# Performance work log

Hardware: AMD Instinct MI355X
Metric: run time of the kernel (lower is better)

The kernel has to match this reference:

```python
import jax, jax.numpy as jnp
import numpy as np

B, T, IN_F, OUT_F = 2, 1024, 1024, 4096
CHUNK = 64  # out_features chunk to bound the (N, CHUNK, IN_F) intermediate


def setup_inputs() -> dict:
    key = jax.random.key(0)
    k1, k2 = jax.random.split(key)
    x = jax.random.normal(k1, (B, T, IN_F), dtype=jnp.float32)
    # torch reset_parameters: uniform_(-0.1, 0.1)
    w = jax.random.uniform(k2, (OUT_F, IN_F), minval=-0.1, maxval=0.1, dtype=jnp.float32)
    b = jnp.zeros((OUT_F,), dtype=jnp.float32)  # bias initialized to zeros
    return {"input": x, "weight_patterns": w, "bias": b}


def reference(input, weight_patterns, bias):
    Bb, Tt, D = input.shape
    x = input.reshape(Bb * Tt, D)  # (N, IN_F)
    n_out = weight_patterns.shape[0]
    w_chunks = weight_patterns.reshape(n_out // CHUNK, CHUNK, D)

    def chunk_fn(w_c):  # w_c: (CHUNK, IN_F)
        # -sum_k |x_nk - w_ck|  -> (N, CHUNK)
        return -jnp.sum(jnp.abs(x[:, None, :] - w_c[None, :, :]), axis=-1)

    out = jax.lax.map(chunk_fn, w_chunks)          # (n_chunks, N, CHUNK)
    out = jnp.transpose(out, (1, 0, 2)).reshape(Bb * Tt, n_out)
    out = out + bias
    return out.reshape(Bb, Tt, n_out)
```

## Files before the change

kernel.cpp:

```cpp
#include <hip/hip_runtime.h>

typedef unsigned int u32;
typedef u32 u32x4 __attribute__((ext_vector_type(4)));
typedef float f32x4 __attribute__((ext_vector_type(4)));

#define N_ROWS 2048
#define K_DIM  1024
#define O_DIM  4096

#define BN 128
#define BO 128
#define KC 128
#define NKT (K_DIM / KC)
#define NTHR 256

#define QSCALE   23.090909f
#define QBIAS    128.5f
#define INVSCALE (5.5f / 127.0f)

__device__ __forceinline__ u32 sad_u8(u32 a, u32 b, u32 c) {
  u32 d;
  asm("v_sad_u8 %0, %1, %2, %3" : "=v"(d) : "v"(a), "v"(b), "v"(c));
  return d;
}

__device__ __forceinline__ u32 quant4(f32x4 v) {
  u32 b0 = (u32)fminf(fmaxf(fmaf(v[0], QSCALE, QBIAS), 0.f), 255.f);
  u32 b1 = (u32)fminf(fmaxf(fmaf(v[1], QSCALE, QBIAS), 0.f), 255.f);
  u32 b2 = (u32)fminf(fmaxf(fmaf(v[2], QSCALE, QBIAS), 0.f), 255.f);
  u32 b3 = (u32)fminf(fmaxf(fmaf(v[3], QSCALE, QBIAS), 0.f), 255.f);
  return b0 | (b1 << 8) | (b2 << 16) | (b3 << 24);
}

__global__ void quant_kernel(const float* __restrict__ src, u32* __restrict__ dst, int n4) {
  int i = blockIdx.x * blockDim.x + threadIdx.x;
  if (i < n4) {
    f32x4 v = ((const f32x4*)src)[i];
    dst[i] = quant4(v);
  }
}

template <bool U8SRC>
__global__ __launch_bounds__(NTHR, 2)
void l1_main(const void* __restrict__ xsrc, const void* __restrict__ wsrc,
             const float* __restrict__ bias, float* __restrict__ out) {
  __shared__ __align__(16) unsigned char lds[2 * 32768];

  const int tid = threadIdx.x;
  const int tx = tid & 15;
  const int ty = tid >> 4;
  const int bo = blockIdx.x & 31;
  const int bn = blockIdx.x >> 5;
  const int n0 = bn * BN, o0 = bo * BO;

  const int srow = tid & 127;
  const int scb = tid >> 7;

  u32x4 xr[4], wr[4];

  u32 acc[8][8];
#pragma unroll
  for (int i = 0; i < 8; ++i)
#pragma unroll
    for (int j = 0; j < 8; ++j) acc[i][j] = 0;

  auto load_tile = [&](int kt) {
    if constexpr (U8SRC) {
      const unsigned char* gx = (const unsigned char*)xsrc +
                                (size_t)(n0 + srow) * K_DIM + kt * KC + scb * 16;
      const unsigned char* gw = (const unsigned char*)wsrc +
                                (size_t)(o0 + srow) * K_DIM + kt * KC + scb * 16;
#pragma unroll
      for (int p = 0; p < 4; ++p) {
        xr[p] = *(const u32x4*)(gx + p * 32);
        wr[p] = *(const u32x4*)(gw + p * 32);
      }
    } else {
      const float* gx = (const float*)xsrc + (size_t)(n0 + srow) * K_DIM + kt * KC + scb * 16;
      const float* gw = (const float*)wsrc + (size_t)(o0 + srow) * K_DIM + kt * KC + scb * 16;
#pragma unroll
      for (int p = 0; p < 4; ++p)
#pragma unroll
        for (int q = 0; q < 4; ++q) {
          xr[p][q] = quant4(*(const f32x4*)(gx + p * 32 + q * 4));
          wr[p][q] = quant4(*(const f32x4*)(gw + p * 32 + q * 4));
        }
    }
  };

  auto write_tile = [&](int p) {
    unsigned char* xl = lds + p * 32768 + scb * 2048 + srow * 16;
    unsigned char* wl = xl + 16384;
#pragma unroll
    for (int q = 0; q < 4; ++q) {
      *(u32x4*)(xl + q * 4096) = xr[q];
      *(u32x4*)(wl + q * 4096) = wr[q];
    }
  };

  auto compute = [&](int p) {
    const unsigned char* xb = lds + p * 32768 + ty * 16;
    const unsigned char* wb = lds + p * 32768 + 16384 + tx * 16;
#pragma unroll
    for (int c = 0; c < 8; ++c) {
      u32x4 xv[8], wv[8];
#pragma unroll
      for (int i = 0; i < 8; ++i) xv[i] = *(const u32x4*)(xb + c * 2048 + i * 256);
#pragma unroll
      for (int j = 0; j < 8; ++j) wv[j] = *(const u32x4*)(wb + c * 2048 + j * 256);
#pragma unroll
      for (int i = 0; i < 8; ++i)
#pragma unroll
        for (int j = 0; j < 8; ++j) {
          acc[i][j] = sad_u8(xv[i][0], wv[j][0], acc[i][j]);
          acc[i][j] = sad_u8(xv[i][1], wv[j][1], acc[i][j]);
          acc[i][j] = sad_u8(xv[i][2], wv[j][2], acc[i][j]);
          acc[i][j] = sad_u8(xv[i][3], wv[j][3], acc[i][j]);
        }
    }
  };

  load_tile(0);
  write_tile(0);
  __syncthreads();

#pragma unroll 1
  for (int kt = 0; kt < NKT; ++kt) {
    if (kt + 1 < NKT) load_tile(kt + 1);
    compute(kt & 1);
    __syncthreads();
    if (kt + 1 < NKT) {
      write_tile((kt + 1) & 1);
      __syncthreads();
    }
  }

  float bj[8];
#pragma unroll
  for (int j = 0; j < 8; ++j) bj[j] = bias[o0 + j * 16 + tx];
#pragma unroll
  for (int i = 0; i < 8; ++i) {
    float* orow = out + (size_t)(n0 + i * 16 + ty) * O_DIM + o0 + tx;
#pragma unroll
    for (int j = 0; j < 8; ++j)
      orow[j * 16] = fmaf((float)acc[i][j], -INVSCALE, bj[j]);
  }
}

extern "C" void kernel_launch(void* const* d_in, const int* in_sizes, int n_in,
                              void* d_out, int out_size, void* d_ws, size_t ws_size,
                              hipStream_t stream) {
  const float* x = (const float*)d_in[0];
  const float* w = (const float*)d_in[1];
  const float* bias = (const float*)d_in[2];
  float* out = (float*)d_out;

  const size_t qx_bytes = (size_t)N_ROWS * K_DIM;
  const size_t qw_bytes = (size_t)O_DIM * K_DIM;

  dim3 grid((N_ROWS / BN) * (O_DIM / BO));
  dim3 block(NTHR);

  if (ws_size >= qx_bytes + qw_bytes) {
    u32* qx = (u32*)d_ws;
    u32* qw = (u32*)((char*)d_ws + qx_bytes);
    int n4x = (int)(qx_bytes / 4);
    int n4w = (int)(qw_bytes / 4);
    quant_kernel<<<(n4x + 255) / 256, 256, 0, stream>>>(x, qx, n4x);
    quant_kernel<<<(n4w + 255) / 256, 256, 0, stream>>>(w, qw, n4w);
    l1_main<true><<<grid, block, 0, stream>>>(qx, qw, bias, out);
  } else {
    l1_main<false><<<grid, block, 0, stream>>>(x, w, bias, out);
  }
}
```

Before: 93.77 us.

## Drop LDS staging; load quantized tiles directly from global with transposed weights

The main kernel no longer stages tiles through LDS with barriers. Each thread reads its x rows and a k-major transposed quantized weight layout straight from global/L1 into double-buffered registers, and writes its outputs as contiguous float4 stores. The weight quantization kernel now produces the transposed layout so weight loads are coalesced across threads. This removes LDS traffic and __syncthreads, but relies on cache hits for the data reused across threads and raises register pressure. The fallback path becomes a naive scalar kernel.

```diff
diff --git a/kernel.cpp b/kernel.cpp
--- a/kernel.cpp
+++ b/kernel.cpp
@@ -6,13 +6,8 @@
 
 #define N_ROWS 2048
 #define K_DIM  1024
+#define K4     256
 #define O_DIM  4096
-
-#define BN 128
-#define BO 128
-#define KC 128
-#define NKT (K_DIM / KC)
-#define NTHR 256
 
 #define QSCALE   23.090909f
 #define QBIAS    128.5f
@@ -32,31 +27,33 @@
   return b0 | (b1 << 8) | (b2 << 16) | (b3 << 24);
 }
 
-__global__ void quant_kernel(const float* __restrict__ src, u32* __restrict__ dst, int n4) {
+__global__ void quant_x_kernel(const float* __restrict__ src, u32* __restrict__ dst, int n4) {
   int i = blockIdx.x * blockDim.x + threadIdx.x;
-  if (i < n4) {
-    f32x4 v = ((const f32x4*)src)[i];
-    dst[i] = quant4(v);
-  }
+  if (i < n4) dst[i] = quant4(((const f32x4*)src)[i]);
 }
 
-template <bool U8SRC>
-__global__ __launch_bounds__(NTHR, 2)
-void l1_main(const void* __restrict__ xsrc, const void* __restrict__ wsrc,
+__global__ void quant_wt_kernel(const float* __restrict__ w, u32* __restrict__ wt) {
+  int t = blockIdx.x * blockDim.x + threadIdx.x;
+  int k4 = t >> 12;
+  int o = t & (O_DIM - 1);
+  wt[t] = quant4(*(const f32x4*)(w + (size_t)o * K_DIM + k4 * 4));
+}
+
+__global__ __launch_bounds__(256, 2)
+void l1_main(const u32* __restrict__ qx, const u32* __restrict__ qwt,
              const float* __restrict__ bias, float* __restrict__ out) {
-  __shared__ __align__(16) unsigned char lds[2 * 32768];
-
   const int tid = threadIdx.x;
   const int tx = tid & 15;
   const int ty = tid >> 4;
   const int bo = blockIdx.x & 31;
   const int bn = blockIdx.x >> 5;
-  const int n0 = bn * BN, o0 = bo * BO;
+  const int n0 = bn * 128, o0 = bo * 128;
+  const int ob = o0 + tx * 8;
 
-  const int srow = tid & 127;
-  const int scb = tid >> 7;
-
-  u32x4 xr[4], wr[4];
+  const u32* xp[8];
+#pragma unroll
+  for (int i = 0; i < 8; ++i) xp[i] = qx + (size_t)(n0 + i * 16 + ty) * K4;
+  const u32* wp = qwt + ob;
 
   u32 acc[8][8];
 #pragma unroll
@@ -64,87 +61,78 @@
 #pragma unroll
     for (int j = 0; j < 8; ++j) acc[i][j] = 0;
 
-  auto load_tile = [&](int kt) {
-    if constexpr (U8SRC) {
-      const unsigned char* gx = (const unsigned char*)xsrc +
-                                (size_t)(n0 + srow) * K_DIM + kt * KC + scb * 16;
-      const unsigned char* gw = (const unsigned char*)wsrc +
-                                (size_t)(o0 + srow) * K_DIM + kt * KC + scb * 16;
+  u32x4 xA[8], wA[8], xB[8], wB[8];
+
+  auto loadx = [&](u32x4(&xb)[8], int c) {
 #pragma unroll
-      for (int p = 0; p < 4; ++p) {
-        xr[p] = *(const u32x4*)(gx + p * 32);
-        wr[p] = *(const u32x4*)(gw + p * 32);
-      }
-    } else {
-      const float* gx = (const float*)xsrc + (size_t)(n0 + srow) * K_DIM + kt * KC + scb * 16;
-      const float* gw = (const float*)wsrc + (size_t)(o0 + srow) * K_DIM + kt * KC + scb * 16;
+    for (int i = 0; i < 8; ++i) xb[i] = *(const u32x4*)(xp[i] + c * 4);
+  };
+  auto loadw = [&](u32x4(&wb)[8], int c) {
 #pragma unroll
-      for (int p = 0; p < 4; ++p)
-#pragma unroll
-        for (int q = 0; q < 4; ++q) {
-          xr[p][q] = quant4(*(const f32x4*)(gx + p * 32 + q * 4));
-          wr[p][q] = quant4(*(const f32x4*)(gw + p * 32 + q * 4));
-        }
+    for (int q = 0; q < 4; ++q) {
+      const u32* p = wp + (size_t)(c * 4 + q) * O_DIM;
+      wb[q * 2] = *(const u32x4*)p;
+      wb[q * 2 + 1] = *(const u32x4*)(p + 4);
     }
   };
-
-  auto write_tile = [&](int p) {
-    unsigned char* xl = lds + p * 32768 + scb * 2048 + srow * 16;
-    unsigned char* wl = xl + 16384;
+  auto dosad = [&](u32x4(&xb)[8], u32x4(&wb)[8]) {
 #pragma unroll
-    for (int q = 0; q < 4; ++q) {
-      *(u32x4*)(xl + q * 4096) = xr[q];
-      *(u32x4*)(wl + q * 4096) = wr[q];
-    }
+    for (int q = 0; q < 4; ++q)
+#pragma unroll
+      for (int i = 0; i < 8; ++i) {
+        u32 xw = xb[i][q];
+        acc[i][0] = sad_u8(xw, wb[q * 2][0], acc[i][0]);
+        acc[i][1] = sad_u8(xw, wb[q * 2][1], acc[i][1]);
+        acc[i][2] = sad_u8(xw, wb[q * 2][2], acc[i][2]);
+        acc[i][3] = sad_u8(xw, wb[q * 2][3], acc[i][3]);
+        acc[i][4] = sad_u8(xw, wb[q * 2 + 1][0], acc[i][4]);
+        acc[i][5] = sad_u8(xw, wb[q * 2 + 1][1], acc[i][5]);
+        acc[i][6] = sad_u8(xw, wb[q * 2 + 1][2], acc[i][6]);
+        acc[i][7] = sad_u8(xw, wb[q * 2 + 1][3], acc[i][7]);
+      }
   };
 
-  auto compute = [&](int p) {
-    const unsigned char* xb = lds + p * 32768 + ty * 16;
-    const unsigned char* wb = lds + p * 32768 + 16384 + tx * 16;
-#pragma unroll
-    for (int c = 0; c < 8; ++c) {
-      u32x4 xv[8], wv[8];
-#pragma unroll
-      for (int i = 0; i < 8; ++i) xv[i] = *(const u32x4*)(xb + c * 2048 + i * 256);
-#pragma unroll
-      for (int j = 0; j < 8; ++j) wv[j] = *(const u32x4*)(wb + c * 2048 + j * 256);
-#pragma unroll
-      for (int i = 0; i < 8; ++i)
-#pragma unroll
-        for (int j = 0; j < 8; ++j) {
-          acc[i][j] = sad_u8(xv[i][0], wv[j][0], acc[i][j]);
-          acc[i][j] = sad_u8(xv[i][1], wv[j][1], acc[i][j]);
-          acc[i][j] = sad_u8(xv[i][2], wv[j][2], acc[i][j]);
-          acc[i][j] = sad_u8(xv[i][3], wv[j][3], acc[i][j]);
-        }
-    }
-  };
-
-  load_tile(0);
-  write_tile(0);
-  __syncthreads();
-
+  loadx(xA, 0); loadw(wA, 0);
+  loadx(xB, 1); loadw(wB, 1);
 #pragma unroll 1
-  for (int kt = 0; kt < NKT; ++kt) {
-    if (kt + 1 < NKT) load_tile(kt + 1);
-    compute(kt & 1);
-    __syncthreads();
-    if (kt + 1 < NKT) {
-      write_tile((kt + 1) & 1);
-      __syncthreads();
-    }
+  for (int c = 0; c < 60; c += 2) {
+    dosad(xA, wA);
+    loadx(xA, c + 2); loadw(wA, c + 2);
+    dosad(xB, wB);
+    loadx(xB, c + 3); loadw(wB, c + 3);
   }
+  dosad(xA, wA); loadx(xA, 62); loadw(wA, 62);
+  dosad(xB, wB); loadx(xB, 63); loadw(wB, 63);
+  dosad(xA, wA);
+  dosad(xB, wB);
 
   float bj[8];
 #pragma unroll
-  for (int j = 0; j < 8; ++j) bj[j] = bias[o0 + j * 16 + tx];
+  for (int j = 0; j < 8; ++j) bj[j] = bias[ob + j];
 #pragma unroll
   for (int i = 0; i < 8; ++i) {
-    float* orow = out + (size_t)(n0 + i * 16 + ty) * O_DIM + o0 + tx;
+    float* op = out + (size_t)(n0 + i * 16 + ty) * O_DIM + ob;
+    f32x4 r0, r1;
 #pragma unroll
-    for (int j = 0; j < 8; ++j)
-      orow[j * 16] = fmaf((float)acc[i][j], -INVSCALE, bj[j]);
+    for (int j = 0; j < 4; ++j) {
+      r0[j] = fmaf((float)acc[i][j], -INVSCALE, bj[j]);
+      r1[j] = fmaf((float)acc[i][j + 4], -INVSCALE, bj[j + 4]);
+    }
+    *(f32x4*)op = r0;
+    *(f32x4*)(op + 4) = r1;
   }
+}
+
+__global__ void l1_fallback(const float* __restrict__ x, const float* __restrict__ w,
+                            const float* __restrict__ bias, float* __restrict__ out) {
+  int t = blockIdx.x * blockDim.x + threadIdx.x;
+  if (t >= N_ROWS * O_DIM) return;
+  int n = t / O_DIM, o = t & (O_DIM - 1);
+  const float* xr = x + (size_t)n * K_DIM;
+  const float* wr = w + (size_t)o * K_DIM;
+  float s = 0.f;
+  for (int k = 0; k < K_DIM; ++k) s += fabsf(xr[k] - wr[k]);
+  out[t] = bias[o] - s;
 }
 
 extern "C" void kernel_launch(void* const* d_in, const int* in_sizes, int n_in,
@@ -158,18 +146,14 @@
   const size_t qx_bytes = (size_t)N_ROWS * K_DIM;
   const size_t qw_bytes = (size_t)O_DIM * K_DIM;
 
-  dim3 grid((N_ROWS / BN) * (O_DIM / BO));
-  dim3 block(NTHR);
-
   if (ws_size >= qx_bytes + qw_bytes) {
     u32* qx = (u32*)d_ws;
-    u32* qw = (u32*)((char*)d_ws + qx_bytes);
+    u32* qwt = (u32*)((char*)d_ws + qx_bytes);
     int n4x = (int)(qx_bytes / 4);
-    int n4w = (int)(qw_bytes / 4);
-    quant_kernel<<<(n4x + 255) / 256, 256, 0, stream>>>(x, qx, n4x);
-    quant_kernel<<<(n4w + 255) / 256, 256, 0, stream>>>(w, qw, n4w);
-    l1_main<true><<<grid, block, 0, stream>>>(qx, qw, bias, out);
+    quant_x_kernel<<<(n4x + 255) / 256, 256, 0, stream>>>(x, qx, n4x);
+    quant_wt_kernel<<<(O_DIM * K4) / 256, 256, 0, stream>>>(w, qwt);
+    l1_main<<<512, 256, 0, stream>>>(qx, qwt, bias, out);
   } else {
-    l1_main<false><<<grid, block, 0, stream>>>(x, w, bias, out);
+    l1_fallback<<<(N_ROWS * O_DIM + 255) / 256, 256, 0, stream>>>(x, w, bias, out);
   }
 }
```

Measured after the change: 96.89 us. 1.03x slower.
